# Kernel optimization log

Measured on AMD Instinct MI355X. Metric: run time of the kernel, lower is better.

The kernel has to match this reference:

```python
import jax, jax.numpy as jnp
import numpy as np

B, S, HID = 2, 1024, 2048
NH, NKV, D = 16, 8, 128
EPS = 1e-4 / 65535.0  # observer eps from ConcatObserver


def _ste(x, dq):
    # straight-through estimator used by torch fake-quant
    return x + jax.lax.stop_gradient(dq - x)


def _fq_range(x, mn, mx):
    # 16-bit per-tensor affine quantize-dequantize over a given range
    scale = jnp.maximum((mx - mn) / 65535.0, EPS)
    zp = jnp.round(-mn / scale)
    q = jnp.clip(jnp.round(x / scale) + zp, 0.0, 65535.0)
    return _ste(x, (q - zp) * scale)


def fq16(x):
    # ActivationQDQ(bits=16), per-tensor affine, zero included in range
    mn = jnp.minimum(jnp.min(x), 0.0)
    mx = jnp.maximum(jnp.max(x), 0.0)
    return _fq_range(x, mn, mx)


def fq8_sym(x):
    # ActivationQDQ(bits=8, per_tensor_symmetric)
    scale = jnp.maximum(jnp.max(jnp.abs(x)) / 127.0, 1e-12)
    q = jnp.clip(jnp.round(x / scale), -128.0, 127.0)
    return _ste(x, q * scale)


def lpbq_linear(x, W, block=32, qmax=7.0):
    # QLinearLPBQ: int4 weights with per-(out, block-of-32-inputs) scales, no bias
    O, I = W.shape
    Wb = W.reshape(O, I // block, block)
    s = jnp.maximum(jnp.max(jnp.abs(Wb), axis=-1, keepdims=True) / qmax, 1e-12)
    Wq = (jnp.clip(jnp.round(Wb / s), -qmax - 1.0, qmax) * s).reshape(O, I)
    return x @ _ste(W, Wq).T


def rmsnorm_fq(x, w, eps=1e-6):
    # QRMSNorm(head_dim, quant_bits=16)
    var = jnp.mean(x * x, axis=-1, keepdims=True)
    return fq16(x * jax.lax.rsqrt(var + eps) * w)


def rotate_half_fq(x):
    # rotate_half with neg-half QDQ and concat observer (range = union of observed tensors)
    d = x.shape[-1] // 2
    x1, x2 = x[..., :d], x[..., d:]
    neg = fq16(-x2)
    mn = jnp.minimum(jnp.minimum(jnp.min(x), jnp.min(neg)), 0.0)
    mx = jnp.maximum(jnp.maximum(jnp.max(x), jnp.max(neg)), 0.0)
    return _fq_range(jnp.concatenate([neg, x1], axis=-1), mn, mx)


def _attn_forward(hidden_states, cos, sin, attention_mask, Wq, Wk, Wv, Wo, q_norm_w, k_norm_w):
    scaling = D ** -0.5
    hs = fq16(hidden_states)                                            # q_proj_input_qdq
    q = fq16(lpbq_linear(hs, Wq)).reshape(B, S, NH, D)                  # q_norm_input_qdq
    q = jnp.transpose(rmsnorm_fq(q, q_norm_w), (0, 2, 1, 3))            # [B,NH,S,D]
    k = fq16(lpbq_linear(hs, Wk)).reshape(B, S, NKV, D)                 # k_norm_input_qdq
    k = jnp.transpose(rmsnorm_fq(k, k_norm_w), (0, 2, 1, 3))            # [B,NKV,S,D]
    v = jnp.transpose(lpbq_linear(hs, Wv).reshape(B, S, NKV, D), (0, 2, 1, 3))
    q = fq16(q)                                                         # q_norm_output_qdq
    k = fq16(k)                                                         # k_norm_output_qdq
    c = cos[:, None, :, :]
    s_ = sin[:, None, :, :]
    q = fq16(fq16(q * c) + fq16(rotate_half_fq(q) * s_))                # q RoPE with QDQs
    k = fq16(fq16(k * c) + fq16(rotate_half_fq(k) * s_))                # k RoPE with QDQs
    k = fq8_sym(k)                                                      # k_cast_to_int8_qdq
    v = fq8_sym(fq16(v))                                                # v int16 then int8 QDQ
    k = jnp.repeat(k, NH // NKV, axis=1)                                # repeat_kv
    v = jnp.repeat(v, NH // NKV, axis=1)
    sc = fq16(jnp.full((1,), scaling, dtype=hs.dtype))                  # scaling_qdq
    attn = fq16(fq16(jnp.einsum('bhsd,bhtd->bhst', q, k)) * sc)         # qk_matmul + mul_0
    amin = fq16(jnp.min(attn, axis=-1, keepdims=True))                  # reduce_min_output_qdq
    vv = fq16(amin + fq16(jnp.full((1,), -20.0, dtype=hs.dtype)))       # minus_0 (+ neg_20)
    attn = fq16(jnp.where(attention_mask == 0, attn, vv))               # where_attn_qdq
    attn = fq16(jax.nn.softmax(attn.astype(jnp.float32), axis=-1).astype(hs.dtype))
    out = fq16(jnp.einsum('bhst,bhtd->bhsd', attn, v))                  # attn_value_matmul
    out = jnp.transpose(out, (0, 2, 1, 3)).reshape(B, S, NH * D)
    return lpbq_linear(out, Wo), attn


def setup_inputs() -> dict:
    key = jax.random.key(0)
    ks = jax.random.split(key, 6)
    hidden_states = jax.random.normal(ks[0], (B, S, HID), jnp.float32)
    pos = jnp.arange(S, dtype=jnp.float32)
    inv_freq = 1.0 / (1e6 ** (jnp.arange(0, D, 2, dtype=jnp.float32) / D))
    fr = pos[:, None] * inv_freq[None, :]
    emb = jnp.concatenate([fr, fr], axis=-1)                            # [S, D]
    cos = jnp.broadcast_to(jnp.cos(emb)[None], (B, S, D))
    sin = jnp.broadcast_to(jnp.sin(emb)[None], (B, S, D))
    attention_mask = jnp.triu(jnp.ones((S, S), jnp.int32), 1)[None, None]  # 0=keep (causal)
    Wq = jax.random.normal(ks[1], (NH * D, HID), jnp.float32) * 0.02
    Wk = jax.random.normal(ks[2], (NKV * D, HID), jnp.float32) * 0.02
    Wv = jax.random.normal(ks[3], (NKV * D, HID), jnp.float32) * 0.02
    Wo = jax.random.normal(ks[4], (HID, NH * D), jnp.float32) * 0.02
    q_norm_w = jnp.ones((D,), jnp.float32)
    k_norm_w = jnp.ones((D,), jnp.float32)
    return {"hidden_states": hidden_states, "cos": cos, "sin": sin,
            "attention_mask": attention_mask, "Wq": Wq, "Wk": Wk, "Wv": Wv, "Wo": Wo,
            "q_norm_w": q_norm_w, "k_norm_w": k_norm_w}


def reference(hidden_states, cos, sin, attention_mask, Wq, Wk, Wv, Wo, q_norm_w, k_norm_w):
    return _attn_forward(hidden_states, cos, sin, attention_mask, Wq, Wk, Wv, Wo, q_norm_w, k_norm_w)
```

## Files before the change

### kernel.cpp

```cpp
#include <hip/hip_runtime.h>
#include <cfloat>
#include <cmath>


#define FQ_EPS      1.5259021896696422e-09f
#define SCALING_F   0.08838834764831845f
#define S_LEN       1024

typedef _Float16 h8_t __attribute__((ext_vector_type(8)));
typedef _Float16 h4_t __attribute__((ext_vector_type(4)));
typedef float    f4_t __attribute__((ext_vector_type(4)));
typedef unsigned short u16x4 __attribute__((ext_vector_type(4)));

__device__ __forceinline__ unsigned f2o(float f){
  unsigned u = __float_as_uint(f);
  return (u & 0x80000000u) ? ~u : (u | 0x80000000u);
}
__device__ __forceinline__ float o2f(unsigned u){
  return __uint_as_float((u & 0x80000000u) ? (u ^ 0x80000000u) : ~u);
}
__device__ __forceinline__ float dec_slot(const unsigned* st, int s){ return o2f(st[s*16]); }

struct FQP { float scale, zp, inv; };
__device__ __forceinline__ FQP fqp_raw(float mn, float mx){
  FQP p; p.scale = fmaxf((mx - mn)/65535.0f, FQ_EPS); p.zp = rintf(-mn/p.scale);
  p.inv = 1.0f/p.scale; return p;
}
__device__ __forceinline__ FQP fqp(float mn0, float mx0){
  return fqp_raw(fminf(mn0, 0.0f), fmaxf(mx0, 0.0f));
}
__device__ __forceinline__ float fqa(float x, FQP p){
  float q = rintf(x*p.inv) + p.zp;
  q = fminf(fmaxf(q, 0.0f), 65535.0f);
  return (q - p.zp)*p.scale;
}
__device__ __forceinline__ float fq8(float x, float s, float si){
  return fminf(fmaxf(rintf(x*si), -128.0f), 127.0f)*s;
}

__device__ __forceinline__ float bred_min(float v, float* red){
  int tid = threadIdx.x; red[tid] = v; __syncthreads();
  for (int s = 128; s > 0; s >>= 1){ if (tid < s) red[tid] = fminf(red[tid], red[tid+s]); __syncthreads(); }
  float r = red[0]; __syncthreads(); return r;
}
__device__ __forceinline__ float bred_max(float v, float* red){
  int tid = threadIdx.x; red[tid] = v; __syncthreads();
  for (int s = 128; s > 0; s >>= 1){ if (tid < s) red[tid] = fmaxf(red[tid], red[tid+s]); __syncthreads(); }
  float r = red[0]; __syncthreads(); return r;
}


__global__ void k_init(unsigned* stats){
  int i = blockIdx.x*blockDim.x + threadIdx.x;
  if (i < 1024) stats[i] = (((i & 15) == 0) && (((i >> 4) & 1) == 0)) ? 0xFFFFFFFFu : 0u;
}

__global__ __launch_bounds__(256) void k_quantw4(const float* __restrict__ Wq, const float* __restrict__ Wk,
                                                 const float* __restrict__ Wv, const float* __restrict__ Wo,
                                                 _Float16* __restrict__ Qh, _Float16* __restrict__ Kh,
                                                 _Float16* __restrict__ Vh, _Float16* __restrict__ Oh,
                                                 const float* __restrict__ hs, unsigned* stats){
  int bx = blockIdx.x;
  if (bx >= 12288){
    float mn = FLT_MAX, mx = -FLT_MAX;
    for (int i = (bx - 12288)*256 + threadIdx.x; i < 4194304; i += 262144){
      float v = hs[i]; mn = fminf(mn, v); mx = fmaxf(mx, v);
    }
    __shared__ float red[256];
    float bmn = bred_min(mn, red), bmx = bred_max(mx, red);
    if (threadIdx.x == 0){ atomicMin(&stats[0], f2o(bmn)); atomicMax(&stats[16], f2o(bmx)); }
    return;
  }
  const float* W; _Float16* Wh; int base;
  if (bx < 4096){ W = Wq; Wh = Qh; base = 0; }
  else if (bx < 6144){ W = Wk; Wh = Kh; base = 4096; }
  else if (bx < 8192){ W = Wv; Wh = Vh; base = 6144; }
  else { W = Wo; Wh = Oh; base = 8192; }
  int i = (bx - base)*256 + threadIdx.x;
  float4 v = ((const float4*)W)[i];
  float am = fmaxf(fmaxf(fabsf(v.x), fabsf(v.y)), fmaxf(fabsf(v.z), fabsf(v.w)));
  #pragma unroll
  for (int m = 1; m < 8; m <<= 1) am = fmaxf(am, __shfl_xor(am, m, 64));
  float s = fmaxf(am/7.0f, 1e-12f), si = 1.0f/s;
  h4_t o;
  o[0] = (_Float16)(fminf(fmaxf(rintf(v.x*si), -8.0f), 7.0f)*s);
  o[1] = (_Float16)(fminf(fmaxf(rintf(v.y*si), -8.0f), 7.0f)*s);
  o[2] = (_Float16)(fminf(fmaxf(rintf(v.z*si), -8.0f), 7.0f)*s);
  o[3] = (_Float16)(fminf(fmaxf(rintf(v.w*si), -8.0f), 7.0f)*s);
  *(h4_t*)(Wh + ((size_t)i << 2)) = o;
}

__global__ __launch_bounds__(256) void k_fq_ew16(const float* __restrict__ x, _Float16* __restrict__ y,
                                                 const unsigned* stats, int slot){
  FQP p = fqp(dec_slot(stats, slot), dec_slot(stats, slot+1));
  int i = blockIdx.x*256 + threadIdx.x;
  float4 v = ((const float4*)x)[i];
  h4_t o;
  o[0] = (_Float16)fqa(v.x, p); o[1] = (_Float16)fqa(v.y, p);
  o[2] = (_Float16)fqa(v.z, p); o[3] = (_Float16)fqa(v.w, p);
  *(h4_t*)(y + ((size_t)i << 2)) = o;
}

__global__ __launch_bounds__(256) void k_fq_qk(const float* __restrict__ qbuf, const float* __restrict__ kbuf,
                                               _Float16* __restrict__ q_h, _Float16* __restrict__ k_h,
                                               const unsigned* stats){
  int bx = blockIdx.x;
  if (bx < 4096){
    FQP p = fqp(dec_slot(stats, 24), dec_slot(stats, 25));
    int i = bx*256 + threadIdx.x;
    float4 v = ((const float4*)qbuf)[i];
    h4_t o;
    o[0] = (_Float16)fqa(v.x, p); o[1] = (_Float16)fqa(v.y, p);
    o[2] = (_Float16)fqa(v.z, p); o[3] = (_Float16)fqa(v.w, p);
    *(h4_t*)(q_h + ((size_t)i << 2)) = o;
  } else {
    FQP p = fqp(dec_slot(stats, 26), dec_slot(stats, 27));
    float lo = fqa(dec_slot(stats, 26), p), hi = fqa(dec_slot(stats, 27), p);
    float s8 = fmaxf(fmaxf(fabsf(lo), fabsf(hi))/127.0f, 1e-12f), s8i = 1.0f/s8;
    int i = (bx - 4096)*256 + threadIdx.x;
    float4 v = ((const float4*)kbuf)[i];
    h4_t o;
    o[0] = (_Float16)fq8(fqa(v.x, p), s8, s8i); o[1] = (_Float16)fq8(fqa(v.y, p), s8, s8i);
    o[2] = (_Float16)fq8(fqa(v.z, p), s8, s8i); o[3] = (_Float16)fq8(fqa(v.w, p), s8, s8i);
    *(h4_t*)(k_h + ((size_t)i << 2)) = o;
  }
}

#define GLDS16(g, l) __builtin_amdgcn_global_load_lds( \
    (__attribute__((address_space(1))) unsigned int*)(g), \
    (__attribute__((address_space(3))) unsigned int*)(l), 16, 0, 0)

__device__ __forceinline__ void stage_tile(const _Float16* __restrict__ src, int ld, int k0,
                                           _Float16* __restrict__ dst){
  #pragma unroll
  for (int it = 0; it < 2; it++){
    int c = threadIdx.x + (it << 8);
    int row = c >> 2, off = (c & 3) << 3;
    GLDS16(src + (size_t)row*ld + k0 + off, dst + (c << 3));
  }
}

__device__ __forceinline__ void hgemm_main64(const _Float16* __restrict__ A, int lda,
                                             const _Float16* __restrict__ B, int ldb, int K,
                                             f4_t acc[4][4], _Float16* As, _Float16* As2,
                                             _Float16* Bs, _Float16* Bs2){
  int lane = threadIdx.x & 63, wave = threadIdx.x >> 6;
  int wm = wave & 1, wn = wave >> 1, quad = lane >> 4, l15 = lane & 15;
  for (int k0 = 0; k0 < K; k0 += 64){
    __syncthreads();
    stage_tile(A, lda, k0, As);
    stage_tile(A, lda, k0 + 32, As2);
    stage_tile(B, ldb, k0, Bs);
    stage_tile(B, ldb, k0 + 32, Bs2);
    __syncthreads();
    #pragma unroll
    for (int half = 0; half < 2; half++){
      const _Float16* Ah = half ? As2 : As;
      const _Float16* Bh = half ? Bs2 : Bs;
      h8_t af[4], bf[4];
      #pragma unroll
      for (int mt = 0; mt < 4; mt++)
        af[mt] = *(const h8_t*)(Ah + ((((wm<<6) + (mt<<4) + l15)) << 5) + (quad << 3));
      #pragma unroll
      for (int nt = 0; nt < 4; nt++)
        bf[nt] = *(const h8_t*)(Bh + ((((wn<<6) + (nt<<4) + l15)) << 5) + (quad << 3));
      #pragma unroll
      for (int mt = 0; mt < 4; mt++)
        #pragma unroll
        for (int nt = 0; nt < 4; nt++)
          acc[mt][nt] = __builtin_amdgcn_mfma_f32_16x16x32_f16(af[mt], bf[nt], acc[mt][nt], 0, 0, 0);
    }
  }
}


__global__ __launch_bounds__(256) void k_hgemm_qkv(const _Float16* __restrict__ A,
                                                   const _Float16* __restrict__ Bq,
                                                   const _Float16* __restrict__ Bk,
                                                   const _Float16* __restrict__ Bv,
                                                   float* __restrict__ Cq, float* __restrict__ Ck,
                                                   float* __restrict__ Cv,
                                                   int K, unsigned* stats){
  __shared__ __align__(16) _Float16 As[4096], As2[4096], Bs[4096], Bs2[4096];
  __shared__ float red[256];
  f4_t acc[4][4];
  { f4_t zz = {0.f,0.f,0.f,0.f};
    for (int i=0;i<4;i++) for (int j=0;j<4;j++) acc[i][j] = zz; }
  int lane = threadIdx.x & 63, wave = threadIdx.x >> 6;
  int wm = wave & 1, wn = wave >> 1, quad = lane >> 4, l15 = lane & 15; (void)lane;
  int z = blockIdx.z;
  const _Float16* Bmat; float* C; int slotC, N, cbase;
  if (z < 2){ Bmat = Bq + (((size_t)z << 10))*K; C = Cq; slotC = 2; N = 2048; cbase = z << 10; }
  else if (z == 2){ Bmat = Bk; C = Ck; slotC = 4; N = 1024; cbase = 0; }
  else { Bmat = Bv; C = Cv; slotC = 6; N = 1024; cbase = 0; }
  int bm = blockIdx.y << 7, bn = blockIdx.x << 7;
  hgemm_main64(A + (size_t)bm*K, K, Bmat + (size_t)bn*K, K, K, acc, As, As2, Bs, Bs2);
  float mn = FLT_MAX, mx = -FLT_MAX;
  #pragma unroll
  for (int mt = 0; mt < 4; mt++)
    #pragma unroll
    for (int nt = 0; nt < 4; nt++){
      int Cc = cbase + bn + (wn<<6) + (nt<<4) + l15;
      #pragma unroll
      for (int i = 0; i < 4; i++){
        int R = bm + (wm<<6) + (mt<<4) + (quad<<2) + i;
        float v = acc[mt][nt][i];
        C[(size_t)R*N + Cc] = v;
        mn = fminf(mn, v); mx = fmaxf(mx, v);
      }
    }
  float bmn = bred_min(mn, red), bmx = bred_max(mx, red);
  if (threadIdx.x == 0){ atomicMin(&stats[slotC*16], f2o(bmn)); atomicMax(&stats[(slotC+1)*16], f2o(bmx)); }
}

__global__ __launch_bounds__(256) void k_hgemm_o(const _Float16* __restrict__ A,
                                                 const _Float16* __restrict__ B,
                                                 float* __restrict__ C){
  __shared__ __align__(16) _Float16 As[4096], As2[4096], Bs[2048], Bs2[2048];
  f4_t acc[4][2];
  { f4_t zz = {0.f,0.f,0.f,0.f};
    for (int i = 0; i < 4; i++) for (int j = 0; j < 2; j++) acc[i][j] = zz; }
  int lane = threadIdx.x & 63, wave = threadIdx.x >> 6;
  int wm = wave & 1, wn = wave >> 1, quad = lane >> 4, l15 = lane & 15;
  int bm = blockIdx.y << 7, bn = blockIdx.x << 6;
  const _Float16* Ab = A + (size_t)bm*2048;
  const _Float16* Bb = B + (size_t)bn*2048;
  for (int k0 = 0; k0 < 2048; k0 += 64){
    __syncthreads();
    stage_tile(Ab, 2048, k0, As);
    stage_tile(Ab, 2048, k0 + 32, As2);
    { int c = threadIdx.x;
      int row = c >> 2, off = (c & 3) << 3;
      GLDS16(Bb + (size_t)row*2048 + k0 + off, Bs + (c << 3));
      GLDS16(Bb + (size_t)row*2048 + k0 + 32 + off, Bs2 + (c << 3)); }
    __syncthreads();
    #pragma unroll
    for (int half = 0; half < 2; half++){
      const _Float16* Ah = half ? As2 : As;
      const _Float16* Bh = half ? Bs2 : Bs;
      h8_t af[4], bf[2];
      #pragma unroll
      for (int mt = 0; mt < 4; mt++)
        af[mt] = *(const h8_t*)(Ah + ((((wm<<6) + (mt<<4) + l15)) << 5) + (quad << 3));
      #pragma unroll
      for (int nt = 0; nt < 2; nt++)
        bf[nt] = *(const h8_t*)(Bh + ((((wn<<5) + (nt<<4) + l15)) << 5) + (quad << 3));
      #pragma unroll
      for (int mt = 0; mt < 4; mt++)
        #pragma unroll
        for (int nt = 0; nt < 2; nt++)
          acc[mt][nt] = __builtin_amdgcn_mfma_f32_16x16x32_f16(af[mt], bf[nt], acc[mt][nt], 0, 0, 0);
    }
  }
  #pragma unroll
  for (int mt = 0; mt < 4; mt++)
    #pragma unroll
    for (int nt = 0; nt < 2; nt++){
      int Cc = bn + (wn<<5) + (nt<<4) + l15;
      #pragma unroll
      for (int i = 0; i < 4; i++){
        int R = bm + (wm<<6) + (mt<<4) + (quad<<2) + i;
        C[(size_t)R*2048 + Cc] = acc[mt][nt][i];
      }
    }
}


#define QK_IDS \
  int lane = threadIdx.x & 63, wn = threadIdx.x >> 6; \
  int quad = lane >> 4, l15 = lane & 15; \
  int tid = threadIdx.x; (void)tid; (void)lane;

__device__ __forceinline__ void qk_load_a(const _Float16* __restrict__ Ab, int quad, int l15,
                                          h8_t Aq[2][4]){
  #pragma unroll
  for (int mt = 0; mt < 2; mt++)
    #pragma unroll
    for (int k0 = 0; k0 < 4; k0++)
      Aq[mt][k0] = *(const h8_t*)(Ab + (size_t)((mt<<4) + l15)*128 + (k0<<5) + (quad<<3));
}

__device__ __forceinline__ void qk_chunk32(const h8_t Aq[2][4], const _Float16* __restrict__ Kb,
                                           int bn, int wn, int quad, int l15, f4_t acc[2][2]){
  #pragma unroll
  for (int k0 = 0; k0 < 4; k0++){
    h8_t bf[2];
    #pragma unroll
    for (int nt = 0; nt < 2; nt++)
      bf[nt] = *(const h8_t*)(Kb + (size_t)(bn + (wn<<5) + (nt<<4) + l15)*128 + (k0<<5) + (quad<<3));
    #pragma unroll
    for (int mt = 0; mt < 2; mt++)
      #pragma unroll
      for (int nt = 0; nt < 2; nt++)
        acc[mt][nt] = __builtin_amdgcn_mfma_f32_16x16x32_f16(Aq[mt][k0], bf[nt], acc[mt][nt], 0, 0, 0);
  }
}

__global__ __launch_bounds__(256) void k_qk_stats(const _Float16* __restrict__ q_h, const _Float16* __restrict__ k_h,
                                                  unsigned* stats, unsigned* rowmin, unsigned* rowmax){
  QK_IDS
  int bm = blockIdx.x << 5, z = blockIdx.y;
  int b = z >> 4, h = z & 15;
  const _Float16* Ab = q_h + (size_t)z*131072 + (size_t)bm*128;
  const _Float16* Kb = k_h + (size_t)(b*8 + (h>>1))*131072;
  h8_t Aq[2][4];
  qk_load_a(Ab, quad, l15, Aq);
  float rmv[2][4], rxa[2][4], rxv[2][4];
  #pragma unroll
  for (int mt = 0; mt < 2; mt++)
    #pragma unroll
    for (int i = 0; i < 4; i++){ rmv[mt][i] = FLT_MAX; rxa[mt][i] = -FLT_MAX; rxv[mt][i] = -FLT_MAX; }
  for (int bn = 0; bn < 1024; bn += 128){
    f4_t acc[2][2];
    { f4_t zz = {0.f,0.f,0.f,0.f}; for (int i=0;i<2;i++) for (int j=0;j<2;j++) acc[i][j]=zz; }
    qk_chunk32(Aq, Kb, bn, wn, quad, l15, acc);
    #pragma unroll
    for (int mt = 0; mt < 2; mt++){
      int rb = bm + (mt<<4) + (quad<<2);
      #pragma unroll
      for (int nt = 0; nt < 2; nt++){
        int t = bn + (wn<<5) + (nt<<4) + l15;
        #pragma unroll
        for (int i = 0; i < 4; i++){
          float v = acc[mt][nt][i];
          rmv[mt][i] = fminf(rmv[mt][i], v);
          rxa[mt][i] = fmaxf(rxa[mt][i], v);
          if (t <= rb + i) rxv[mt][i] = fmaxf(rxv[mt][i], v);
        }
      }
    }
  }
  #pragma unroll
  for (int d = 1; d < 16; d <<= 1)
    #pragma unroll
    for (int mt = 0; mt < 2; mt++)
      #pragma unroll
      for (int i = 0; i < 4; i++){
        rmv[mt][i] = fminf(rmv[mt][i], __shfl_xor(rmv[mt][i], d, 64));
        rxa[mt][i] = fmaxf(rxa[mt][i], __shfl_xor(rxa[mt][i], d, 64));
        rxv[mt][i] = fmaxf(rxv[mt][i], __shfl_xor(rxv[mt][i], d, 64));
      }
  __shared__ float rminS[4][32], rmaxS[4][32];
  if (l15 == 0){
    #pragma unroll
    for (int mt = 0; mt < 2; mt++)
      #pragma unroll
      for (int i = 0; i < 4; i++){
        int rl = (mt<<4) + (quad<<2) + i;
        rminS[wn][rl] = rmv[mt][i];
        rmaxS[wn][rl] = rxv[mt][i];
      }
  }
  __syncthreads();
  if (tid < 32){
    float a = fminf(fminf(rminS[0][tid], rminS[1][tid]), fminf(rminS[2][tid], rminS[3][tid]));
    float c = fmaxf(fmaxf(rmaxS[0][tid], rmaxS[1][tid]), fmaxf(rmaxS[2][tid], rmaxS[3][tid]));
    rowmin[(z << 10) + bm + tid] = f2o(a);
    rowmax[(z << 10) + bm + tid] = f2o(c);
    float am = a;
    #pragma unroll
    for (int d = 1; d < 32; d <<= 1) am = fmaxf(am, __shfl_xor(am, d, 32));
    if (tid == 0) atomicMax(&stats[35*16], f2o(am));
  }
  float mn = FLT_MAX, mx = -FLT_MAX, mxU = -FLT_MAX;
  #pragma unroll
  for (int mt = 0; mt < 2; mt++)
    #pragma unroll
    for (int i = 0; i < 4; i++){
      mn = fminf(mn, rmv[mt][i]);
      mx = fmaxf(mx, rxa[mt][i]);
      mxU = fmaxf(mxU, rxv[mt][i]);
    }
  __shared__ float red[256];
  float bmn = bred_min(mn, red), bmx = bred_max(mx, red), bmU = bred_max(mxU, red);
  if (tid == 0){
    atomicMin(&stats[28*16], f2o(bmn));
    atomicMax(&stats[29*16], f2o(bmx));
    atomicMax(&stats[31*16], f2o(bmU));
  }
}

struct LogitQ { FQP f1, f2, fam, fvv, f3; float sc, c20; };
__device__ LogitQ derive_logit(const unsigned* st){
  LogitQ L;
  FQP ps = fqp(SCALING_F, SCALING_F); L.sc = fqa(SCALING_F, ps);
  FQP p20 = fqp(-20.0f, -20.0f);      L.c20 = fqa(-20.0f, p20);
  float gmn = dec_slot(st, 28), gmx = dec_slot(st, 29);
  float gU = dec_slot(st, 31), M2 = dec_slot(st, 35);
  L.f1 = fqp(gmn, gmx);
  float l1lo = fqa(gmn, L.f1), l1hi = fqa(gmx, L.f1);
  L.f2 = fqp(l1lo*L.sc, l1hi*L.sc);
  float amlo = fqa(fqa(gmn, L.f1)*L.sc, L.f2);
  float amhi = fqa(fqa(M2, L.f1)*L.sc, L.f2);
  L.fam = fqp(amlo, amhi);
  float vslo = fqa(amlo, L.fam) + L.c20, vshi = fqa(amhi, L.fam) + L.c20;
  L.fvv = fqp(vslo, vshi);
  float mn3 = fqa(vslo, L.fvv);
  float mx3 = fqa(fqa(gU, L.f1)*L.sc, L.f2);
  L.f3 = fqp(mn3, mx3);
  return L;
}
__device__ __forceinline__ float chainU(float raw, const LogitQ& L){
  return fqa(fqa(fqa(raw, L.f1)*L.sc, L.f2), L.f3);
}

__global__ __launch_bounds__(256) void k_qk_denom(const _Float16* __restrict__ q_h, const _Float16* __restrict__ k_h,
                                                  const unsigned* __restrict__ rowmin,
                                                  const unsigned* __restrict__ rowmax,
                                                  float* __restrict__ denomS,
                                                  unsigned short* __restrict__ q3buf,
                                                  unsigned* stats){
  QK_IDS
  int j = blockIdx.x, z = blockIdx.y;
  int b = z >> 4, h = z & 15;
  LogitQ L = derive_logit(stats);
  const _Float16* Kb = k_h + (size_t)(b*8 + (h>>1))*131072;
  __shared__ float mRow[32], vvRow[32], vvLev[32];
  __shared__ float dS[4][32];
  for (int g = 0; g < 2; g++){
    int r = g ? (31 - j) : j;
    int bm = r << 5;
    int nch = (r >> 2) + 1;
    int cstar = (r >> 2) << 7;
    int aa = r >> 2, bb2 = r & 3;
    int cum = (aa + 1)*(2*aa + bb2);
    unsigned short* Qu = q3buf + ((size_t)z*144 + cum)*4096;
    __syncthreads();
    if (tid < 32){
      int row = (z << 10) + bm + tid;
      mRow[tid] = chainU(o2f(rowmax[row]), L);
      float tr = fqa(fqa(o2f(rowmin[row]), L.f1)*L.sc, L.f2);
      float w = fqa(fqa(tr, L.fam) + L.c20, L.fvv);
      float lv = fminf(fmaxf(rintf(w*L.f3.inv) + L.f3.zp, 0.0f), 65535.0f);
      vvLev[tid] = lv;
      vvRow[tid] = (lv - L.f3.zp)*L.f3.scale;
    }
    const _Float16* Ab = q_h + (size_t)z*131072 + (size_t)bm*128;
    h8_t Aq[2][4];
    qk_load_a(Ab, quad, l15, Aq);
    __syncthreads();
    float rs[2][4];
    #pragma unroll
    for (int mt = 0; mt < 2; mt++)
      #pragma unroll
      for (int i = 0; i < 4; i++) rs[mt][i] = 0.0f;
    for (int bn = 0; bn < (nch << 7); bn += 128){
      f4_t acc[2][2];
      { f4_t zz = {0.f,0.f,0.f,0.f}; for (int i=0;i<2;i++) for (int jj=0;jj<2;jj++) acc[i][jj]=zz; }
      qk_chunk32(Aq, Kb, bn, wn, quad, l15, acc);
      unsigned short* Qc = Qu + (size_t)(bn >> 7)*4096;
      if (bn < cstar){
        #pragma unroll
        for (int mt = 0; mt < 2; mt++){
          #pragma unroll
          for (int nt = 0; nt < 2; nt++){
            int cl = (wn<<5) + (nt<<4) + l15;
            #pragma unroll
            for (int i = 0; i < 4; i++){
              int rl = (mt<<4) + (quad<<2) + i;
              float a2 = fqa(fqa(acc[mt][nt][i], L.f1)*L.sc, L.f2);
// ... 60 lines not shown
  int j = blockIdx.x, z = blockIdx.y;
  int b = z >> 4, h = z & 15;
  LogitQ L = derive_logit(stats);
  FQP p4 = fqp(0.0f, 1.0f/dec_slot(stats, 32));
  float c1024 = p4.scale*1024.0f;
  float p4s = p4.scale;
  float zp3 = L.f3.zp, s3 = L.f3.scale;
  const _Float16* Vb = vT + (size_t)(b*8 + (h>>1))*131072;
  float* Cb = ctx + ((size_t)b << 10)*2048 + (size_t)h*128;
  float cmn = FLT_MAX, cmx = -FLT_MAX;
  for (int g = 0; g < 2; g++){
    int r = g ? (31 - j) : j;
    int bm = r << 5;
    int nch = (r >> 2) + 1;
    int aa = r >> 2, bb2 = r & 3;
    int cum = (aa + 1)*(2*aa + bb2);
    const unsigned short* Qu = q3buf + ((size_t)z*144 + cum)*4096;
    float* Ap = attn + ((size_t)z << 20) + (size_t)bm*1024;
    float mR[2], rpR[2];
    #pragma unroll
    for (int mt = 0; mt < 2; mt++){
      int row = (z << 10) + bm + (mt<<4) + l15;
      mR[mt] = chainU(o2f(rowmax[row]), L);
      rpR[mt] = p4.inv/denomS[row];
    }
    f4_t pacc[2][2];
    { f4_t zz = {0.f,0.f,0.f,0.f}; for (int i=0;i<2;i++) for (int jj=0;jj<2;jj++) pacc[i][jj]=zz; }
    for (int c = 0; c < nch; c++){
      const unsigned short* Qc = Qu + (size_t)c*4096;
      #pragma unroll
      for (int k0 = 0; k0 < 4; k0++){
        h8_t af[2], bf[2];
        #pragma unroll
        for (int mt = 0; mt < 2; mt++){
          const unsigned short* pr = Qc + ((mt<<4) + l15)*128 + (k0<<5) + (quad<<3);
          u16x4 u = *(const u16x4*)pr, w = *(const u16x4*)(pr + 4);
          h8_t o;
          f4_t va, vb;
          #pragma unroll
          for (int jj = 0; jj < 4; jj++){
            float a3u = ((float)u[jj] - zp3)*s3;
            float nu = fminf(fmaxf(rintf(__expf(a3u - mR[mt])*rpR[mt]), 0.0f), 65535.0f);
            o[jj] = (_Float16)(nu*c1024);
            va[jj] = nu*p4s;
            float a3w = ((float)w[jj] - zp3)*s3;
            float nw = fminf(fmaxf(rintf(__expf(a3w - mR[mt])*rpR[mt]), 0.0f), 65535.0f);
            o[jj+4] = (_Float16)(nw*c1024);
            vb[jj] = nw*p4s;
          }
          af[mt] = o;
          float* ap = Ap + (size_t)((mt<<4) + l15)*1024 + (c<<7) + (k0<<5) + (quad<<3);
          *(f4_t*)ap = va;
          *(f4_t*)(ap + 4) = vb;
        }
        #pragma unroll
        for (int nt = 0; nt < 2; nt++)
          bf[nt] = *(const h8_t*)(Vb + (size_t)((wn<<5) + (nt<<4) + l15)*1024 + (c<<7) + (k0<<5) + (quad<<3));
        #pragma unroll
        for (int mt = 0; mt < 2; mt++)
          #pragma unroll
          for (int nt = 0; nt < 2; nt++)
            pacc[mt][nt] = __builtin_amdgcn_mfma_f32_16x16x32_f16(af[mt], bf[nt], pacc[mt][nt], 0, 0, 0);
      }
    }
    #pragma unroll
    for (int mt = 0; mt < 2; mt++)
      #pragma unroll
      for (int nt = 0; nt < 2; nt++){
        int Cc = (wn<<5) + (nt<<4) + l15;
        #pragma unroll
        for (int i = 0; i < 4; i++){
          int R = bm + (mt<<4) + (quad<<2) + i;
          float v = pacc[mt][nt][i]*(1.0f/1024.0f);
          Cb[(size_t)R*2048 + Cc] = v;
          cmn = fminf(cmn, v); cmx = fmaxf(cmx, v);
        }
      }
  }
  __shared__ float red[256];
  float bmn = bred_min(cmn, red), bmx = bred_max(cmx, red);
  if (tid == 0){ atomicMin(&stats[36*16], f2o(bmn)); atomicMax(&stats[37*16], f2o(bmx)); }
}

__global__ __launch_bounds__(256) void k_attn_zero(float* __restrict__ attn){
  int j = blockIdx.x, z = blockIdx.y;
  int lane = threadIdx.x & 63, wn = threadIdx.x >> 6;
  f4_t zz = {0.f,0.f,0.f,0.f};
  #pragma unroll
  for (int g = 0; g < 2; g++){
    int r = g ? (31 - j) : j;
    int nch = (r >> 2) + 1;
    int col0 = nch << 7;
    if (col0 >= 1024) continue;
    float* Cb = attn + ((size_t)z << 20) + ((size_t)(r << 5))*1024;
    for (int rr = wn; rr < 32; rr += 4){
      float* rowp = Cb + (size_t)rr*1024;
      for (int c = col0 + (lane << 2); c < 1024; c += 256)
        __builtin_nontemporal_store(zz, (f4_t*)(rowp + c));
    }
  }
}


__global__ __launch_bounds__(256) void k_rms(const float* __restrict__ lin, float* __restrict__ buf,
                                             const float* __restrict__ gw, unsigned* stats,
                                             int slot_lin, int slot_out, int NHh, int rows){
  FQP pA = fqp(dec_slot(stats, slot_lin), dec_slot(stats, slot_lin+1));
  int lane = threadIdx.x & 63;
  int wv = (blockIdx.x*256 + threadIdx.x) >> 6;
  int nwv = (gridDim.x*256) >> 6;
  float w0 = gw[lane], w1 = gw[lane + 64];
  float fmn = FLT_MAX, fmx = -FLT_MAX, hmn = FLT_MAX, hmx = -FLT_MAX;
  for (int r = wv; r < rows; r += nwv){
    int h = r % NHh; int rem = r / NHh; int s2 = rem & 1023; int b = rem >> 10;
    const float* src = lin + (size_t)r*128;
    float x0 = fqa(src[lane], pA), x1 = fqa(src[lane + 64], pA);
    float ss = x0*x0 + x1*x1;
    #pragma unroll
    for (int m = 1; m < 64; m <<= 1) ss += __shfl_xor(ss, m, 64);
    float rr = 1.0f/sqrtf(ss*(1.0f/128.0f) + 1e-6f);
    float y0 = x0*rr*w0, y1 = x1*rr*w1;
    float* dst = buf + ((size_t)((b*NHh + h) << 10) + s2)*128;
    dst[lane] = y0; dst[lane + 64] = y1;
    fmn = fminf(fmn, fminf(y0, y1)); fmx = fmaxf(fmx, fmaxf(y0, y1));
    hmn = fminf(hmn, y1); hmx = fmaxf(hmx, y1);
  }
  __shared__ float red[256];
  float a = bred_min(fmn, red), bb = bred_max(fmx, red);
  float c = bred_min(hmn, red), d = bred_max(hmx, red);
  if (threadIdx.x == 0){
    atomicMin(&stats[slot_out*16], f2o(a));     atomicMax(&stats[(slot_out+1)*16], f2o(bb));
    atomicMin(&stats[(slot_out+2)*16], f2o(c)); atomicMax(&stats[(slot_out+3)*16], f2o(d));
  }
}

struct RopeQ { FQP B, C, E, F; };
__device__ RopeQ derive_rope(const unsigned* st, int base){
  float ymn = dec_slot(st, base),   ymx = dec_slot(st, base+1);
  float y2mn = dec_slot(st, base+2), y2mx = dec_slot(st, base+3);
  RopeQ r;
  r.B = fqp(ymn, ymx);
  float zmn = fqa(ymn, r.B), zmx = fqa(ymx, r.B);
  r.C = fqp(zmn, zmx);
  float zlo = fqa(zmn, r.C), zhi = fqa(zmx, r.C);
  float z2lo = fqa(fqa(y2mn, r.B), r.C), z2hi = fqa(fqa(y2mx, r.B), r.C);
  r.E = fqp(-z2hi, -z2lo);
  float nlo = fqa(-z2hi, r.E), nhi = fqa(-z2lo, r.E);
  r.F = fqp_raw(fminf(fminf(zlo, nlo), 0.0f), fmaxf(fmaxf(zhi, nhi), 0.0f));
  return r;
}

__global__ __launch_bounds__(256) void k_rope(float* __restrict__ bufq, float* __restrict__ bufk,
                                              const float* __restrict__ cosp, const float* __restrict__ sinp,
                                              unsigned* stats, int do_write){
  int isK = (blockIdx.x >= 1024);
  float* buf = isK ? bufk : bufq;
  int slot_norm = isK ? 12 : 8, slot_prod = isK ? 20 : 16, slot_sum = isK ? 26 : 24;
  int NHh = isK ? 8 : 16, rows = isK ? 16384 : 32768;
  int bid = isK ? (blockIdx.x - 1024) : blockIdx.x;
  int nblk = isK ? 512 : 1024;
  RopeQ R = derive_rope(stats, slot_norm);
  FQP pD, pG;
  if (do_write){
    pD = fqp(dec_slot(stats, slot_prod),   dec_slot(stats, slot_prod+1));
    pG = fqp(dec_slot(stats, slot_prod+2), dec_slot(stats, slot_prod+3));
  }
  int lane = threadIdx.x & 63;
  int wv = (bid*256 + threadIdx.x) >> 6, nwv = (nblk*256) >> 6;
  float m0 = FLT_MAX, M0 = -FLT_MAX, m1 = FLT_MAX, M1 = -FLT_MAX;
  for (int r = wv; r < rows; r += nwv){
    int s2 = r & 1023; int bh = r >> 10; int b = bh/NHh;
    float* base = buf + (size_t)r*128;
    float y0 = base[lane], y1 = base[lane + 64];
    float z0 = fqa(fqa(y0, R.B), R.C), z1 = fqa(fqa(y1, R.B), R.C);
    const float* cr = cosp + (size_t)((b << 10) + s2)*128;
    const float* sr = sinp + (size_t)((b << 10) + s2)*128;
    float c0 = cr[lane], c1 = cr[lane + 64], sn0 = sr[lane], sn1 = sr[lane + 64];
    float pc0 = z0*c0, pc1 = z1*c1;
    float rh0 = fqa(fqa(-z1, R.E), R.F);
    float rh1 = fqa(z0, R.F);
    float ps0 = rh0*sn0, ps1 = rh1*sn1;
    if (!do_write){
      m0 = fminf(m0, fminf(pc0, pc1)); M0 = fmaxf(M0, fmaxf(pc0, pc1));
      m1 = fminf(m1, fminf(ps0, ps1)); M1 = fmaxf(M1, fmaxf(ps0, ps1));
    } else {
      float sv0 = fqa(pc0, pD) + fqa(ps0, pG);
      float sv1 = fqa(pc1, pD) + fqa(ps1, pG);
      base[lane] = sv0; base[lane + 64] = sv1;
      m0 = fminf(m0, fminf(sv0, sv1)); M0 = fmaxf(M0, fmaxf(sv0, sv1));
    }
  }
  __shared__ float red[256];
  if (!do_write){
    float a = bred_min(m0, red), bb = bred_max(M0, red);
    float c = bred_min(m1, red), d = bred_max(M1, red);
    if (threadIdx.x == 0){
      atomicMin(&stats[slot_prod*16], f2o(a));     atomicMax(&stats[(slot_prod+1)*16], f2o(bb));
      atomicMin(&stats[(slot_prod+2)*16], f2o(c)); atomicMax(&stats[(slot_prod+3)*16], f2o(d));
    }
  } else {
    float a = bred_min(m0, red), bb = bred_max(M0, red);
    if (threadIdx.x == 0){ atomicMin(&stats[slot_sum*16], f2o(a)); atomicMax(&stats[(slot_sum+1)*16], f2o(bb)); }
  }
}

__global__ __launch_bounds__(256) void k_vT(const float* __restrict__ vlin, _Float16* __restrict__ vT,
                                            const unsigned* stats){
  FQP pv = fqp(dec_slot(stats, 6), dec_slot(stats, 7));
  float vlo = fqa(dec_slot(stats, 6), pv), vhi = fqa(dec_slot(stats, 7), pv);
  float v8s = fmaxf(fmaxf(fabsf(vlo), fabsf(vhi))/127.0f, 1e-12f), v8si = 1.0f/v8s;
  __shared__ float tile[64][65];
  int bkv = blockIdx.z, t0 = blockIdx.x << 6, d0 = blockIdx.y << 6;
  int b = bkv >> 3, kv = bkv & 7;
  const float* src = vlin + ((size_t)(b << 10))*1024 + (size_t)kv*128;
  int tx = threadIdx.x & 63, tq = threadIdx.x >> 6;
  #pragma unroll
  for (int i = 0; i < 16; i++){
    int tt = (i << 2) + tq;
    float x = src[(size_t)(t0 + tt)*1024 + d0 + tx];
    tile[tx][tt] = fq8(fqa(x, pv), v8s, v8si);
  }
  __syncthreads();
  _Float16* dst = vT + (size_t)bkv*131072;
  #pragma unroll
  for (int i = 0; i < 16; i++){
    int dd = (i << 2) + tq;
    dst[(size_t)(d0 + dd)*1024 + t0 + tx] = (_Float16)tile[dd][tx];
  }
}

extern "C" void kernel_launch(void* const* d_in, const int* in_sizes, int n_in,
                              void* d_out, int out_size, void* d_ws, size_t ws_size,
                              hipStream_t stream){
  (void)in_sizes; (void)n_in; (void)out_size; (void)ws_size;
  const float* hs   = (const float*)d_in[0];
  const float* cosp = (const float*)d_in[1];
  const float* sinp = (const float*)d_in[2];
  const float* Wq   = (const float*)d_in[4];
  const float* Wk   = (const float*)d_in[5];
  const float* Wv   = (const float*)d_in[6];
  const float* Wo   = (const float*)d_in[7];
  const float* qnw  = (const float*)d_in[8];
  const float* knw  = (const float*)d_in[9];

  float* outp = (float*)d_out;
  float* attn = outp + 4194304;

  const size_t MEG = 1u << 20;
  float* wsf = (float*)d_ws;
  _Float16* woq_h = (_Float16*)(wsf + 0);
  _Float16* wqq_h = (_Float16*)(wsf + 2*MEG);
  _Float16* wkq_h = (_Float16*)(wsf + 4*MEG);
  _Float16* wvq_h = (_Float16*)(wsf + 5*MEG);
  _Float16* hsq_h = (_Float16*)(wsf + 6*MEG);
  float* qlin = wsf + 8*MEG;  float* ctx = qlin;
  float* klin = wsf + 12*MEG;
  float* vlin = wsf + 14*MEG;
  float* qbuf = wsf + 16*MEG;
  float* kbuf = wsf + 20*MEG;
  _Float16* q_h   = (_Float16*)(wsf + 22*MEG);
  _Float16* k_h   = (_Float16*)(wsf + 24*MEG);
  _Float16* vT_h  = (_Float16*)(wsf + 25*MEG);
  _Float16* ctx_h = (_Float16*)(wsf + 26*MEG);
  unsigned* rowmin = (unsigned*)(wsf + 28*MEG);
  unsigned* rowmax = (unsigned*)(wsf + 28*MEG + 32768);
  float* denomS = wsf + 28*MEG + 65536;
  unsigned* stats = (unsigned*)(wsf + 28*MEG + 98304);
  unsigned short* q3buf = (unsigned short*)(wsf + 12*MEG);

  k_init<<<4, 256, 0, stream>>>(stats);

  k_quantw4<<<13312, 256, 0, stream>>>(Wq, Wk, Wv, Wo, wqq_h, wkq_h, wvq_h, woq_h, hs, stats);

  k_fq_ew16<<<4096, 256, 0, stream>>>(hs, hsq_h, stats, 0);

  k_hgemm_qkv<<<dim3(8, 16, 4), 256, 0, stream>>>(hsq_h, wqq_h, wkq_h, wvq_h,
                                                  qlin, klin, vlin, 2048, stats);

  k_rms<<<1024, 256, 0, stream>>>(qlin, qbuf, qnw, stats, 2, 8, 16, 32768);
  k_rms<<<512, 256, 0, stream>>>(klin, kbuf, knw, stats, 4, 12, 8, 16384);

  k_rope<<<1536, 256, 0, stream>>>(qbuf, kbuf, cosp, sinp, stats, 0);
  k_rope<<<1536, 256, 0, stream>>>(qbuf, kbuf, cosp, sinp, stats, 1);

  k_fq_qk<<<6144, 256, 0, stream>>>(qbuf, kbuf, q_h, k_h, stats);
  k_vT<<<dim3(16, 2, 16), 256, 0, stream>>>(vlin, vT_h, stats);

  k_qk_stats<<<dim3(32, 32), 256, 0, stream>>>(q_h, k_h, stats, rowmin, rowmax);
  k_qk_denom<<<dim3(16, 32), 256, 0, stream>>>(q_h, k_h, rowmin, rowmax, denomS, q3buf, stats);
  k_qk_pv<<<dim3(16, 32), 256, 0, stream>>>(q3buf, vT_h, ctx, attn, rowmax, denomS, stats);
  k_attn_zero<<<dim3(16, 32), 256, 0, stream>>>(attn);

  k_fq_ew16<<<4096, 256, 0, stream>>>(ctx, ctx_h, stats, 36);
  k_hgemm_o<<<dim3(32, 16), 256, 0, stream>>>(ctx_h, woq_h, outp);
}
```

Baseline: 589.6 us.

## Merge small kernels, shrink QKV GEMM N-tile, split QK stats loop by causal region

```diff
diff --git a/kernel.cpp b/kernel.cpp
--- a/kernel.cpp
+++ b/kernel.cpp
@@ -101,9 +101,12 @@
   *(h4_t*)(y + ((size_t)i << 2)) = o;
 }
 
-__global__ __launch_bounds__(256) void k_fq_qk(const float* __restrict__ qbuf, const float* __restrict__ kbuf,
-                                               _Float16* __restrict__ q_h, _Float16* __restrict__ k_h,
-                                               const unsigned* stats){
+__global__ __launch_bounds__(256) void k_fq_qk_vt(const float* __restrict__ qbuf, const float* __restrict__ kbuf,
+                                                  const float* __restrict__ vlin,
+                                                  _Float16* __restrict__ q_h, _Float16* __restrict__ k_h,
+                                                  _Float16* __restrict__ vT,
+                                                  const unsigned* stats){
+  __shared__ float tile[64][65];
   int bx = blockIdx.x;
   if (bx < 4096){
     FQP p = fqp(dec_slot(stats, 24), dec_slot(stats, 25));
@@ -113,7 +116,7 @@
     o[0] = (_Float16)fqa(v.x, p); o[1] = (_Float16)fqa(v.y, p);
     o[2] = (_Float16)fqa(v.z, p); o[3] = (_Float16)fqa(v.w, p);
     *(h4_t*)(q_h + ((size_t)i << 2)) = o;
-  } else {
+  } else if (bx < 6144){
     FQP p = fqp(dec_slot(stats, 26), dec_slot(stats, 27));
     float lo = fqa(dec_slot(stats, 26), p), hi = fqa(dec_slot(stats, 27), p);
     float s8 = fmaxf(fmaxf(fabsf(lo), fabsf(hi))/127.0f, 1e-12f), s8i = 1.0f/s8;
@@ -123,6 +126,28 @@
     o[0] = (_Float16)fq8(fqa(v.x, p), s8, s8i); o[1] = (_Float16)fq8(fqa(v.y, p), s8, s8i);
     o[2] = (_Float16)fq8(fqa(v.z, p), s8, s8i); o[3] = (_Float16)fq8(fqa(v.w, p), s8, s8i);
     *(h4_t*)(k_h + ((size_t)i << 2)) = o;
+  } else {
+    int idx = bx - 6144;
+    int t0 = (idx & 15) << 6, d0 = ((idx >> 4) & 1) << 6, bkv = idx >> 5;
+    FQP pv = fqp(dec_slot(stats, 6), dec_slot(stats, 7));
+    float vlo = fqa(dec_slot(stats, 6), pv), vhi = fqa(dec_slot(stats, 7), pv);
+    float v8s = fmaxf(fmaxf(fabsf(vlo), fabsf(vhi))/127.0f, 1e-12f), v8si = 1.0f/v8s;
+    int b = bkv >> 3, kv = bkv & 7;
+    const float* src = vlin + ((size_t)(b << 10))*1024 + (size_t)kv*128;
+    int tx = threadIdx.x & 63, tq = threadIdx.x >> 6;
+    #pragma unroll
+    for (int i = 0; i < 16; i++){
+      int tt = (i << 2) + tq;
+      float x = src[(size_t)(t0 + tt)*1024 + d0 + tx];
+      tile[tx][tt] = fq8(fqa(x, pv), v8s, v8si);
+    }
+    __syncthreads();
+    _Float16* dst = vT + (size_t)bkv*131072;
+    #pragma unroll
+    for (int i = 0; i < 16; i++){
+      int dd = (i << 2) + tq;
+      dst[(size_t)(d0 + dd)*1024 + t0 + tx] = (_Float16)tile[dd][tx];
+    }
   }
 }
 
@@ -140,39 +165,6 @@
   }
 }
 
-__device__ __forceinline__ void hgemm_main64(const _Float16* __restrict__ A, int lda,
-                                             const _Float16* __restrict__ B, int ldb, int K,
-                                             f4_t acc[4][4], _Float16* As, _Float16* As2,
-                                             _Float16* Bs, _Float16* Bs2){
-  int lane = threadIdx.x & 63, wave = threadIdx.x >> 6;
-  int wm = wave & 1, wn = wave >> 1, quad = lane >> 4, l15 = lane & 15;
-  for (int k0 = 0; k0 < K; k0 += 64){
-    __syncthreads();
-    stage_tile(A, lda, k0, As);
-    stage_tile(A, lda, k0 + 32, As2);
-    stage_tile(B, ldb, k0, Bs);
-    stage_tile(B, ldb, k0 + 32, Bs2);
-    __syncthreads();
-    #pragma unroll
-    for (int half = 0; half < 2; half++){
-      const _Float16* Ah = half ? As2 : As;
-      const _Float16* Bh = half ? Bs2 : Bs;
-      h8_t af[4], bf[4];
-      #pragma unroll
-      for (int mt = 0; mt < 4; mt++)
-        af[mt] = *(const h8_t*)(Ah + ((((wm<<6) + (mt<<4) + l15)) << 5) + (quad << 3));
-      #pragma unroll
-      for (int nt = 0; nt < 4; nt++)
-        bf[nt] = *(const h8_t*)(Bh + ((((wn<<6) + (nt<<4) + l15)) << 5) + (quad << 3));
-      #pragma unroll
-      for (int mt = 0; mt < 4; mt++)
-        #pragma unroll
-        for (int nt = 0; nt < 4; nt++)
-          acc[mt][nt] = __builtin_amdgcn_mfma_f32_16x16x32_f16(af[mt], bf[nt], acc[mt][nt], 0, 0, 0);
-    }
-  }
-}
-
 
 __global__ __launch_bounds__(256) void k_hgemm_qkv(const _Float16* __restrict__ A,
                                                    const _Float16* __restrict__ Bq,
@@ -181,26 +173,54 @@
                                                    float* __restrict__ Cq, float* __restrict__ Ck,
                                                    float* __restrict__ Cv,
                                                    int K, unsigned* stats){
-  __shared__ __align__(16) _Float16 As[4096], As2[4096], Bs[4096], Bs2[4096];
+  __shared__ __align__(16) _Float16 As[4096], As2[4096], Bs[2048], Bs2[2048];
   __shared__ float red[256];
-  f4_t acc[4][4];
+  f4_t acc[4][2];
   { f4_t zz = {0.f,0.f,0.f,0.f};
-    for (int i=0;i<4;i++) for (int j=0;j<4;j++) acc[i][j] = zz; }
+    for (int i = 0; i < 4; i++) for (int j = 0; j < 2; j++) acc[i][j] = zz; }
   int lane = threadIdx.x & 63, wave = threadIdx.x >> 6;
-  int wm = wave & 1, wn = wave >> 1, quad = lane >> 4, l15 = lane & 15; (void)lane;
+  int wm = wave & 1, wn = wave >> 1, quad = lane >> 4, l15 = lane & 15;
   int z = blockIdx.z;
   const _Float16* Bmat; float* C; int slotC, N, cbase;
   if (z < 2){ Bmat = Bq + (((size_t)z << 10))*K; C = Cq; slotC = 2; N = 2048; cbase = z << 10; }
   else if (z == 2){ Bmat = Bk; C = Ck; slotC = 4; N = 1024; cbase = 0; }
   else { Bmat = Bv; C = Cv; slotC = 6; N = 1024; cbase = 0; }
-  int bm = blockIdx.y << 7, bn = blockIdx.x << 7;
-  hgemm_main64(A + (size_t)bm*K, K, Bmat + (size_t)bn*K, K, K, acc, As, As2, Bs, Bs2);
+  int bm = blockIdx.y << 7, bn = blockIdx.x << 6;
+  const _Float16* Ab = A + (size_t)bm*K;
+  const _Float16* Bb = Bmat + (size_t)bn*K;
+  for (int k0 = 0; k0 < K; k0 += 64){
+    __syncthreads();
+    stage_tile(Ab, K, k0, As);
+    stage_tile(Ab, K, k0 + 32, As2);
+    { int c = threadIdx.x;
+      int row = c >> 2, off = (c & 3) << 3;
+      GLDS16(Bb + (size_t)row*K + k0 + off, Bs + (c << 3));
+      GLDS16(Bb + (size_t)row*K + k0 + 32 + off, Bs2 + (c << 3)); }
+    __syncthreads();
+    #pragma unroll
+    for (int half = 0; half < 2; half++){
+      const _Float16* Ah = half ? As2 : As;
+      const _Float16* Bh = half ? Bs2 : Bs;
+      h8_t af[4], bf[2];
+      #pragma unroll
+      for (int mt = 0; mt < 4; mt++)
+        af[mt] = *(const h8_t*)(Ah + ((((wm<<6) + (mt<<4) + l15)) << 5) + (quad << 3));
+      #pragma unroll
+      for (int nt = 0; nt < 2; nt++)
+        bf[nt] = *(const h8_t*)(Bh + ((((wn<<5) + (nt<<4) + l15)) << 5) + (quad << 3));
+      #pragma unroll
+      for (int mt = 0; mt < 4; mt++)
+        #pragma unroll
+        for (int nt = 0; nt < 2; nt++)
+          acc[mt][nt] = __builtin_amdgcn_mfma_f32_16x16x32_f16(af[mt], bf[nt], acc[mt][nt], 0, 0, 0);
+    }
+  }
   float mn = FLT_MAX, mx = -FLT_MAX;
   #pragma unroll
   for (int mt = 0; mt < 4; mt++)
     #pragma unroll
-    for (int nt = 0; nt < 4; nt++){
-      int Cc = cbase + bn + (wn<<6) + (nt<<4) + l15;
+    for (int nt = 0; nt < 2; nt++){
+      int Cc = cbase + bn + (wn<<5) + (nt<<4) + l15;
       #pragma unroll
       for (int i = 0; i < 4; i++){
         int R = bm + (wm<<6) + (mt<<4) + (quad<<2) + i;
@@ -297,39 +317,91 @@
 }
 
 __global__ __launch_bounds__(256) void k_qk_stats(const _Float16* __restrict__ q_h, const _Float16* __restrict__ k_h,
-                                                  unsigned* stats, unsigned* rowmin, unsigned* rowmax){
+                                                  unsigned* stats, unsigned* rowmin, unsigned* rowmax,
+                                                  float* __restrict__ attn){
   QK_IDS
-  int bm = blockIdx.x << 5, z = blockIdx.y;
+  int z = blockIdx.y;
+  if (blockIdx.x >= 32){
+    int j = blockIdx.x - 32;
+    f4_t zz = {0.f,0.f,0.f,0.f};
+    #pragma unroll
+    for (int g = 0; g < 2; g++){
+      int r = g ? (31 - j) : j;
+      int nch = (r >> 2) + 1;
+      int col0 = nch << 7;
+      if (col0 >= 1024) continue;
+      float* Cb = attn + ((size_t)z << 20) + ((size_t)(r << 5))*1024;
+      for (int rr = wn; rr < 32; rr += 4){
+        float* rowp = Cb + (size_t)rr*1024;
+        for (int c = col0 + (lane << 2); c < 1024; c += 256)
+          __builtin_nontemporal_store(zz, (f4_t*)(rowp + c));
+      }
+    }
+    return;
+  }
+  int bm = blockIdx.x << 5;
   int b = z >> 4, h = z & 15;
+  int cstar = (blockIdx.x >> 2) << 7;
   const _Float16* Ab = q_h + (size_t)z*131072 + (size_t)bm*128;
   const _Float16* Kb = k_h + (size_t)(b*8 + (h>>1))*131072;
   h8_t Aq[2][4];
   qk_load_a(Ab, quad, l15, Aq);
-  float rmv[2][4], rxa[2][4], rxv[2][4];
+  float rmv[2][4], rxv[2][4], rxm[2][4];
   #pragma unroll
   for (int mt = 0; mt < 2; mt++)
     #pragma unroll
-    for (int i = 0; i < 4; i++){ rmv[mt][i] = FLT_MAX; rxa[mt][i] = -FLT_MAX; rxv[mt][i] = -FLT_MAX; }
-  for (int bn = 0; bn < 1024; bn += 128){
+    for (int i = 0; i < 4; i++){ rmv[mt][i] = FLT_MAX; rxv[mt][i] = -FLT_MAX; rxm[mt][i] = -FLT_MAX; }
+  for (int bn = 0; bn < cstar; bn += 128){
     f4_t acc[2][2];
     { f4_t zz = {0.f,0.f,0.f,0.f}; for (int i=0;i<2;i++) for (int j=0;j<2;j++) acc[i][j]=zz; }
     qk_chunk32(Aq, Kb, bn, wn, quad, l15, acc);
     #pragma unroll
-    for (int mt = 0; mt < 2; mt++){
-      int rb = bm + (mt<<4) + (quad<<2);
-      #pragma unroll
-      for (int nt = 0; nt < 2; nt++){
-        int t = bn + (wn<<5) + (nt<<4) + l15;
+    for (int mt = 0; mt < 2; mt++)
+      #pragma unroll
+      for (int nt = 0; nt < 2; nt++)
         #pragma unroll
         for (int i = 0; i < 4; i++){
           float v = acc[mt][nt][i];
           rmv[mt][i] = fminf(rmv[mt][i], v);
-          rxa[mt][i] = fmaxf(rxa[mt][i], v);
+          rxv[mt][i] = fmaxf(rxv[mt][i], v);
+        }
+  }
+  {
+    int bn = cstar;
+    f4_t acc[2][2];
+    { f4_t zz = {0.f,0.f,0.f,0.f}; for (int i=0;i<2;i++) for (int j=0;j<2;j++) acc[i][j]=zz; }
+    qk_chunk32(Aq, Kb, bn, wn, quad, l15, acc);
+    #pragma unroll
+    for (int mt = 0; mt < 2; mt++){
+      int rb = bm + (mt<<4) + (quad<<2);
+      #pragma unroll
+      for (int nt = 0; nt < 2; nt++){
+        int t = bn + (wn<<5) + (nt<<4) + l15;
+        #pragma unroll
+        for (int i = 0; i < 4; i++){
+          float v = acc[mt][nt][i];
+          rmv[mt][i] = fminf(rmv[mt][i], v);
           if (t <= rb + i) rxv[mt][i] = fmaxf(rxv[mt][i], v);
+          else             rxm[mt][i] = fmaxf(rxm[mt][i], v);
         }
       }
     }
   }
+  for (int bn = cstar + 128; bn < 1024; bn += 128){
+    f4_t acc[2][2];
+    { f4_t zz = {0.f,0.f,0.f,0.f}; for (int i=0;i<2;i++) for (int j=0;j<2;j++) acc[i][j]=zz; }
+    qk_chunk32(Aq, Kb, bn, wn, quad, l15, acc);
+    #pragma unroll
+    for (int mt = 0; mt < 2; mt++)
+      #pragma unroll
+      for (int nt = 0; nt < 2; nt++)
+        #pragma unroll
+        for (int i = 0; i < 4; i++){
+          float v = acc[mt][nt][i];
+          rmv[mt][i] = fminf(rmv[mt][i], v);
+          rxm[mt][i] = fmaxf(rxm[mt][i], v);
+        }
+  }
   #pragma unroll
   for (int d = 1; d < 16; d <<= 1)
     #pragma unroll
@@ -337,8 +409,8 @@
       #pragma unroll
       for (int i = 0; i < 4; i++){
         rmv[mt][i] = fminf(rmv[mt][i], __shfl_xor(rmv[mt][i], d, 64));
-        rxa[mt][i] = fmaxf(rxa[mt][i], __shfl_xor(rxa[mt][i], d, 64));
         rxv[mt][i] = fmaxf(rxv[mt][i], __shfl_xor(rxv[mt][i], d, 64));
+        rxm[mt][i] = fmaxf(rxm[mt][i], __shfl_xor(rxm[mt][i], d, 64));
       }
   __shared__ float rminS[4][32], rmaxS[4][32];
   if (l15 == 0){
@@ -362,20 +434,20 @@
     for (int d = 1; d < 32; d <<= 1) am = fmaxf(am, __shfl_xor(am, d, 32));
     if (tid == 0) atomicMax(&stats[35*16], f2o(am));
   }
-  float mn = FLT_MAX, mx = -FLT_MAX, mxU = -FLT_MAX;
+  float mn = FLT_MAX, mxU = -FLT_MAX, mxM = -FLT_MAX;
   #pragma unroll
   for (int mt = 0; mt < 2; mt++)
     #pragma unroll
     for (int i = 0; i < 4; i++){
       mn = fminf(mn, rmv[mt][i]);
-      mx = fmaxf(mx, rxa[mt][i]);
       mxU = fmaxf(mxU, rxv[mt][i]);
+      mxM = fmaxf(mxM, rxm[mt][i]);
     }
   __shared__ float red[256];
-  float bmn = bred_min(mn, red), bmx = bred_max(mx, red), bmU = bred_max(mxU, red);
+  float bmn = bred_min(mn, red), bmU = bred_max(mxU, red), bmM = bred_max(mxM, red);
   if (tid == 0){
     atomicMin(&stats[28*16], f2o(bmn));
-    atomicMax(&stats[29*16], f2o(bmx));
+    atomicMax(&stats[29*16], f2o(fmaxf(bmU, bmM)));
     atomicMax(&stats[31*16], f2o(bmU));
   }
 }
@@ -602,33 +674,23 @@
   if (tid == 0){ atomicMin(&stats[36*16], f2o(bmn)); atomicMax(&stats[37*16], f2o(bmx)); }
 }
 
-__global__ __launch_bounds__(256) void k_attn_zero(float* __restrict__ attn){
-  int j = blockIdx.x, z = blockIdx.y;
-  int lane = threadIdx.x & 63, wn = threadIdx.x >> 6;
-  f4_t zz = {0.f,0.f,0.f,0.f};
-  #pragma unroll
-  for (int g = 0; g < 2; g++){
-    int r = g ? (31 - j) : j;
-    int nch = (r >> 2) + 1;
-    int col0 = nch << 7;
-    if (col0 >= 1024) continue;
-    float* Cb = attn + ((size_t)z << 20) + ((size_t)(r << 5))*1024;
-    for (int rr = wn; rr < 32; rr += 4){
-      float* rowp = Cb + (size_t)rr*1024;
-      for (int c = col0 + (lane << 2); c < 1024; c += 256)
-        __builtin_nontemporal_store(zz, (f4_t*)(rowp + c));
-    }
-  }
-}
-
-
-__global__ __launch_bounds__(256) void k_rms(const float* __restrict__ lin, float* __restrict__ buf,
-                                             const float* __restrict__ gw, unsigned* stats,
-                                             int slot_lin, int slot_out, int NHh, int rows){
+
+__global__ __launch_bounds__(256) void k_rms2(const float* __restrict__ qlin, float* __restrict__ qbuf,
+                                              const float* __restrict__ qnw,
+                                              const float* __restrict__ klin, float* __restrict__ kbuf,
+                                              const float* __restrict__ knw, unsigned* stats){
+  int isK = (blockIdx.x >= 1024);
+  const float* lin = isK ? klin : qlin;
+  float* buf = isK ? kbuf : qbuf;
+  const float* gw = isK ? knw : qnw;
+  int slot_lin = isK ? 4 : 2, slot_out = isK ? 12 : 8;
+  int NHh = isK ? 8 : 16, rows = isK ? 16384 : 32768;
+  int bid = isK ? (blockIdx.x - 1024) : blockIdx.x;
+  int nblk = isK ? 512 : 1024;
   FQP pA = fqp(dec_slot(stats, slot_lin), dec_slot(stats, slot_lin+1));
   int lane = threadIdx.x & 63;
-  int wv = (blockIdx.x*256 + threadIdx.x) >> 6;
-  int nwv = (gridDim.x*256) >> 6;
+  int wv = (bid*256 + threadIdx.x) >> 6;
+  int nwv = (nblk*256) >> 6;
   float w0 = gw[lane], w1 = gw[lane + 64];
   float fmn = FLT_MAX, fmx = -FLT_MAX, hmn = FLT_MAX, hmx = -FLT_MAX;
   for (int r = wv; r < rows; r += nwv){
@@ -724,31 +786,6 @@
   }
 }
 
-__global__ __launch_bounds__(256) void k_vT(const float* __restrict__ vlin, _Float16* __restrict__ vT,
-                                            const unsigned* stats){
-  FQP pv = fqp(dec_slot(stats, 6), dec_slot(stats, 7));
-  float vlo = fqa(dec_slot(stats, 6), pv), vhi = fqa(dec_slot(stats, 7), pv);
-  float v8s = fmaxf(fmaxf(fabsf(vlo), fabsf(vhi))/127.0f, 1e-12f), v8si = 1.0f/v8s;
-  __shared__ float tile[64][65];
-  int bkv = blockIdx.z, t0 = blockIdx.x << 6, d0 = blockIdx.y << 6;
-  int b = bkv >> 3, kv = bkv & 7;
-  const float* src = vlin + ((size_t)(b << 10))*1024 + (size_t)kv*128;
-  int tx = threadIdx.x & 63, tq = threadIdx.x >> 6;
-  #pragma unroll
-  for (int i = 0; i < 16; i++){
-    int tt = (i << 2) + tq;
-    float x = src[(size_t)(t0 + tt)*1024 + d0 + tx];
-    tile[tx][tt] = fq8(fqa(x, pv), v8s, v8si);
-  }
-  __syncthreads();
-  _Float16* dst = vT + (size_t)bkv*131072;
-  #pragma unroll
-  for (int i = 0; i < 16; i++){
-    int dd = (i << 2) + tq;
-    dst[(size_t)(d0 + dd)*1024 + t0 + tx] = (_Float16)tile[dd][tx];
-  }
-}
-
 extern "C" void kernel_launch(void* const* d_in, const int* in_sizes, int n_in,
                               void* d_out, int out_size, void* d_ws, size_t ws_size,
                               hipStream_t stream){
@@ -794,22 +831,19 @@
 
   k_fq_ew16<<<4096, 256, 0, stream>>>(hs, hsq_h, stats, 0);
 
-  k_hgemm_qkv<<<dim3(8, 16, 4), 256, 0, stream>>>(hsq_h, wqq_h, wkq_h, wvq_h,
-                                                  qlin, klin, vlin, 2048, stats);
-
-  k_rms<<<1024, 256, 0, stream>>>(qlin, qbuf, qnw, stats, 2, 8, 16, 32768);
-  k_rms<<<512, 256, 0, stream>>>(klin, kbuf, knw, stats, 4, 12, 8, 16384);
+  k_hgemm_qkv<<<dim3(16, 16, 4), 256, 0, stream>>>(hsq_h, wqq_h, wkq_h, wvq_h,
+                                                   qlin, klin, vlin, 2048, stats);
+
+  k_rms2<<<1536, 256, 0, stream>>>(qlin, qbuf, qnw, klin, kbuf, knw, stats);
 
   k_rope<<<1536, 256, 0, stream>>>(qbuf, kbuf, cosp, sinp, stats, 0);
   k_rope<<<1536, 256, 0, stream>>>(qbuf, kbuf, cosp, sinp, stats, 1);
 
-  k_fq_qk<<<6144, 256, 0, stream>>>(qbuf, kbuf, q_h, k_h, stats);
-  k_vT<<<dim3(16, 2, 16), 256, 0, stream>>>(vlin, vT_h, stats);
-
-  k_qk_stats<<<dim3(32, 32), 256, 0, stream>>>(q_h, k_h, stats, rowmin, rowmax);
+  k_fq_qk_vt<<<6656, 256, 0, stream>>>(qbuf, kbuf, vlin, q_h, k_h, vT_h, stats);
+
+  k_qk_stats<<<dim3(48, 32), 256, 0, stream>>>(q_h, k_h, stats, rowmin, rowmax, attn);
   k_qk_denom<<<dim3(16, 32), 256, 0, stream>>>(q_h, k_h, rowmin, rowmax, denomS, q3buf, stats);
   k_qk_pv<<<dim3(16, 32), 256, 0, stream>>>(q3buf, vT_h, ctx, attn, rowmax, denomS, stats);
-  k_attn_zero<<<dim3(16, 32), 256, 0, stream>>>(attn);
 
   k_fq_ew16<<<4096, 256, 0, stream>>>(ctx, ctx_h, stats, 36);
   k_hgemm_o<<<dim3(32, 16), 256, 0, stream>>>(ctx_h, woq_h, outp);
```

Result: faster. 553.5 us, median of 2 (-6.1%).
